# Performance work log

Hardware: AMD Instinct MI355X
Metric: run time of the kernel (lower is better)

Reference implementation:

```python
import jax, jax.numpy as jnp
import numpy as np

N_USERS = 50000
N_ENT = 100000
N_EDGES = 2_000_000
N_INTER = 1_000_000
CHANNEL = 64
N_HEADS = 2
D_K = CHANNEL // N_HEADS
N_HOPS = 2
N_REL = 10  # relation_emb has N_REL-1 rows


def setup_inputs() -> dict:
    key = jax.random.key(0)
    ks = jax.random.split(key, 8)
    user_emb = jax.random.normal(ks[0], (N_USERS, CHANNEL), jnp.float32) * 0.1
    entity_emb = jax.random.normal(ks[1], (N_ENT, CHANNEL), jnp.float32) * 0.1
    relation_emb = jax.random.normal(ks[2], (N_REL - 1, CHANNEL), jnp.float32) * 0.1
    W_Q = jax.random.normal(ks[3], (CHANNEL, CHANNEL), jnp.float32) * (1.0 / np.sqrt(CHANNEL))
    edge_index = jax.random.randint(ks[4], (2, N_EDGES), 0, N_ENT)
    edge_type = jax.random.randint(ks[5], (N_EDGES,), 1, N_REL)  # in [1, N_REL-1]
    inter_edge = jnp.stack([
        jax.random.randint(ks[6], (N_INTER,), 0, N_USERS),
        jax.random.randint(ks[7], (N_INTER,), 0, N_ENT),
    ])
    inter_edge_w = jnp.full((N_INTER,), 1.0 / 20.0, jnp.float32)
    return {
        "user_emb": user_emb,
        "entity_emb": entity_emb,
        "relation_emb": relation_emb,
        "W_Q": W_Q,
        "inter_edge_w": inter_edge_w,
        "edge_index": edge_index,
        "edge_type": edge_type,
        "inter_edge": inter_edge,
    }


def _l2norm(x):
    # F.normalize(dim=-1) with eps=1e-12
    n = jnp.linalg.norm(x, axis=-1, keepdims=True)
    return x / jnp.maximum(n, 1e-12)


def _scatter_softmax(logits, seg, num_segments):
    # per-segment (over leading axis) numerically-stable softmax; logits [E, H]
    m = jax.ops.segment_max(logits, seg, num_segments=num_segments)
    e = jnp.exp(logits - m[seg])
    s = jax.ops.segment_sum(e, seg, num_segments=num_segments)
    return e / s[seg]


def reference(user_emb, entity_emb, relation_emb, W_Q, inter_edge_w,
              edge_index, edge_type, inter_edge):
    head, tail = edge_index[0], edge_index[1]
    u_idx, i_idx = inter_edge[0], inter_edge[1]
    rel = relation_emb[edge_type - 1]  # [E, C]
    inv_sqrt_dk = 1.0 / np.sqrt(D_K)

    entity_res, user_res = entity_emb, user_emb
    for _ in range(N_HOPS):
        h_emb = entity_emb[head]                       # [E, C]
        t_emb = entity_emb[tail]                       # [E, C]
        q = (h_emb @ W_Q).reshape(-1, N_HEADS, D_K)    # [E, H, Dk]
        k = (t_emb @ W_Q).reshape(-1, N_HEADS, D_K) * rel.reshape(-1, N_HEADS, D_K)
        score = (q * k).sum(-1) * inv_sqrt_dk          # [E, H]
        attn = _scatter_softmax(score, head, N_ENT)    # [E, H]
        value = (t_emb * rel).reshape(-1, N_HEADS, D_K)
        agg = (value * attn[..., None]).reshape(-1, CHANNEL)
        entity_agg = jax.ops.segment_sum(agg, head, num_segments=N_ENT)
        item_agg = inter_edge_w[:, None] * entity_emb[i_idx]
        user_agg = jax.ops.segment_sum(item_agg, u_idx, num_segments=N_USERS)
        # mess_dropout disabled (eval mode)
        entity_emb = _l2norm(entity_agg)
        user_emb = _l2norm(user_agg)
        entity_res = entity_res + entity_emb
        user_res = user_res + user_emb
    return entity_res, user_res
```

## Files before the change

### kernel.cpp

```cpp
#include <hip/hip_runtime.h>

#define NU     50000
#define NEN    100000
#define NEDGE  2000000
#define NINTER 1000000
#define CH     64
#define NRELM1 9
#define CAPE   64
#define CAPU   64

#define BINSH   8
#define NBINE   ((NEN + 255) >> BINSH)
#define NBINU   ((NU  + 255) >> BINSH)
#define CHUNKE  4096
#define CHUNKU  2048
#define NBE_BLK ((NEDGE  + CHUNKE - 1) / CHUNKE)
#define NBU_BLK ((NINTER + CHUNKU - 1) / CHUNKU)
#define DSTRE   416
#define DSTRU   224
#define NSTR_E  ((NEN * CH) / 2048)
#define NSTR_U  ((NU * CH + 2047) / 2048)
#define NPLACE  (NBINE + NBINU)
#define NGEMM0  ((NEN + 127) / 128)
#define NGEMM   ((NEN + 63) / 64)

typedef _Float16 hv2 __attribute__((ext_vector_type(2)));
typedef _Float16 h8  __attribute__((ext_vector_type(8)));
typedef float    f32x4 __attribute__((ext_vector_type(4)));
union P4 { float4 f; hv2 h[4]; };

static __device__ __forceinline__ hv2 pkrtz(float a, float b) {
    return __builtin_bit_cast(hv2, __builtin_amdgcn_cvt_pkrtz(a, b));
}


__global__ __launch_bounds__(256) void k_bin(
    const float* __restrict__ ue, const float* __restrict__ ee,
    const float* __restrict__ re, const float* __restrict__ wq,
    const float* __restrict__ iw, const int* __restrict__ eidx,
    const int* __restrict__ etype, const int* __restrict__ ii,
    _Float16* __restrict__ QE, float* __restrict__ Eres, float* __restrict__ Ures,
    _Float16* __restrict__ Relh, _Float16* __restrict__ Wt,
    unsigned* __restrict__ dirE, unsigned* __restrict__ dirU,
    int* __restrict__ blkBufE, unsigned long long* __restrict__ blkBufU)
{
    __shared__ long long srt64[CHUNKU];
    __shared__ int hist[512];
    __shared__ int sc[512];
    __shared__ int segtot[8];
    int* srt = (int*)srt64;
    int b = blockIdx.x, tid = threadIdx.x;
    int lane63 = tid & 63, wv = tid >> 6;

    if (b < NBE_BLK) {
        hist[tid] = 0; hist[tid + 256] = 0;
        __syncthreads();
        int base = b * CHUNKE;
        int n = NEDGE - base; if (n > CHUNKE) n = CHUNKE;
        for (int i = tid; i < n; i += 256)
            atomicAdd(&hist[eidx[base + i] >> BINSH], 1);
        __syncthreads();
        {
            int v0 = hist[tid], v1 = hist[tid + 256];
            int s0 = v0, s1 = v1;
#pragma unroll
            for (int off = 1; off < 64; off <<= 1) {
                int u0 = __shfl_up(s0, off);
                int u1 = __shfl_up(s1, off);
                if (lane63 >= off) { s0 += u0; s1 += u1; }
            }
            if (lane63 == 63) { segtot[wv] = s0; segtot[4 + wv] = s1; }
            __syncthreads();
            int base0 = 0, base1 = 0;
#pragma unroll
            for (int k = 0; k < 8; ++k) {
                int t = segtot[k];
                if (k < wv)     base0 += t;
                if (k < 4 + wv) base1 += t;
            }
            sc[tid]       = base0 + s0 - v0;
            sc[tid + 256] = base1 + s1 - v1;
            __syncthreads();
        }
        for (int i = tid; i < n; i += 256) {
            int h  = eidx[base + i];
            int t  = eidx[NEDGE + base + i];
            int rt = etype[base + i] - 1;
            int pos = atomicAdd(&sc[h >> BINSH], 1);
            srt[pos] = (h & 255) | ((t | (rt << 17)) << 8);
        }
        __syncthreads();
        int4* dst = (int4*)(blkBufE + b * CHUNKE);
        const int4* s4 = (const int4*)srt;
        for (int j = tid; j < ((n + 3) >> 2); j += 256) dst[j] = s4[j];
        for (int bin = tid; bin < NBINE; bin += 256)
            dirE[b * DSTRE + bin] =
                ((unsigned)(sc[bin] - hist[bin]) << 16) | (unsigned)hist[bin];
    } else if (b < NBE_BLK + NBU_BLK) {
        hist[tid] = 0; hist[tid + 256] = 0;
        __syncthreads();
        int ub = b - NBE_BLK;
        int base = ub * CHUNKU;
        int n = NINTER - base; if (n > CHUNKU) n = CHUNKU;
        for (int i = tid; i < n; i += 256)
            atomicAdd(&hist[ii[base + i] >> BINSH], 1);
        __syncthreads();
        {
            int v0 = hist[tid], v1 = hist[tid + 256];
            int s0 = v0, s1 = v1;
#pragma unroll
            for (int off = 1; off < 64; off <<= 1) {
                int u0 = __shfl_up(s0, off);
                int u1 = __shfl_up(s1, off);
                if (lane63 >= off) { s0 += u0; s1 += u1; }
            }
            if (lane63 == 63) { segtot[wv] = s0; segtot[4 + wv] = s1; }
            __syncthreads();
            int base0 = 0, base1 = 0;
#pragma unroll
            for (int k = 0; k < 8; ++k) {
                int t = segtot[k];
                if (k < wv)     base0 += t;
                if (k < 4 + wv) base1 += t;
            }
            sc[tid]       = base0 + s0 - v0;
            sc[tid + 256] = base1 + s1 - v1;
            __syncthreads();
        }
        for (int i = tid; i < n; i += 256) {
            int u = ii[base + i];
            int e = ii[NINTER + base + i];
            unsigned w = __float_as_uint(iw[base + i]);
            int pos = atomicAdd(&sc[u >> BINSH], 1);
            srt64[pos] = (unsigned long long)((u & 255) | (e << 8))
                       | ((unsigned long long)w << 32);
        }
        __syncthreads();
        int4* dst = (int4*)(blkBufU + (size_t)ub * CHUNKU);
        const int4* s4 = (const int4*)srt64;
        for (int j = tid; j < ((n + 1) >> 1); j += 256) dst[j] = s4[j];
        for (int bin = tid; bin < NBINU; bin += 256)
            dirU[ub * DSTRU + bin] =
                ((unsigned)(sc[bin] - hist[bin]) << 16) | (unsigned)hist[bin];
    } else {
        int sb = b - (NBE_BLK + NBU_BLK);
        if (sb < NSTR_E) {
            int i0 = sb * 2048 + tid * 8;
            float4 a = *(const float4*)(ee + i0);
            float4 c = *(const float4*)(ee + i0 + 4);
            *(float4*)(Eres + i0)     = a;
            *(float4*)(Eres + i0 + 4) = c;
            P4 o;
            o.h[0] = pkrtz(a.x, a.y);
            o.h[1] = pkrtz(a.z, a.w);
            o.h[2] = pkrtz(c.x, c.y);
            o.h[3] = pkrtz(c.z, c.w);
            int node = i0 >> 6, c0 = i0 & 63;
            *(float4*)(QE + (size_t)node * 128 + c0) = o.f;
        } else if (sb < NSTR_E + NSTR_U) {
            int i0 = (sb - NSTR_E) * 2048 + tid * 8;
            if (i0 < NU * CH) {
                *(float4*)(Ures + i0)     = *(const float4*)(ue + i0);
                *(float4*)(Ures + i0 + 4) = *(const float4*)(ue + i0 + 4);
            }
        } else {
            for (int i = tid; i < NRELM1 * CH; i += 256)
                Relh[i] = (_Float16)re[i];
            for (int i = tid; i < CH * CH; i += 256)
                Wt[(i & 63) * 64 + (i >> 6)] = (_Float16)wq[i];
        }
    }
}

__global__ __launch_bounds__(512) void k_pg(
    const unsigned* __restrict__ dirE, const int* __restrict__ blkBufE,
    const unsigned* __restrict__ dirU, const unsigned long long* __restrict__ blkBufU,
    int* __restrict__ cntE, int* __restrict__ csrE,
    int* __restrict__ cntU, unsigned long long* __restrict__ csrU2,
    _Float16* __restrict__ QE, const _Float16* __restrict__ Wt)
{
    __shared__ int cnt[256];
    int b = blockIdx.x, tid = threadIdx.x;
    if (b >= NPLACE) {
        int gb = b - NPLACE;
        int w = tid >> 6, lane = tid & 63;
        int r0 = gb * 128 + w * 16;
        if (r0 >= NEN) return;
        int lr = lane & 15, lg = lane >> 4;
        const _Float16* arow = QE + (size_t)(r0 + lr) * 128 + lg * 8;
        h8 a0 = *(const h8*)(arow);
        h8 a1 = *(const h8*)(arow + 32);
#pragma unroll
        for (int ct = 0; ct < 4; ++ct) {
            const _Float16* brow = Wt + (ct * 16 + lr) * 64 + lg * 8;
            h8 b0 = *(const h8*)(brow);
            h8 b1 = *(const h8*)(brow + 32);
            f32x4 c = {0.f, 0.f, 0.f, 0.f};
            c = __builtin_amdgcn_mfma_f32_16x16x32_f16(a0, b0, c, 0, 0, 0);
            c = __builtin_amdgcn_mfma_f32_16x16x32_f16(a1, b1, c, 0, 0, 0);
#pragma unroll
            for (int r = 0; r < 4; ++r)
                QE[(size_t)(r0 + lg * 4 + r) * 128 + 64 + ct * 16 + lr] = (_Float16)c[r];
        }
        return;
    }
    if (tid < 256) cnt[tid] = 0;
    __syncthreads();
    if (b < NBINE) {
        if (tid < NBE_BLK) {
            unsigned d = dirE[tid * DSTRE + b];
            int off = d >> 16, c = d & 0xFFFF;
            const int* src = blkBufE + tid * CHUNKE + off;
            for (int i = 0; i < c; ++i) {
                int rec = src[i];
                int nl = rec & 255;
                int pos = atomicAdd(&cnt[nl], 1);
                if (pos < CAPE) csrE[((b << BINSH) + nl) * CAPE + pos] = rec >> 8;
            }
        }
        __syncthreads();
        if (tid < 256) {
            int node = (b << BINSH) + tid;
            if (node < NEN) { int c = cnt[tid]; cntE[node] = c > CAPE ? CAPE : c; }
        }
    } else {
        int ub = b - NBINE;
        if (tid < NBU_BLK) {
            unsigned d = dirU[tid * DSTRU + ub];
            int off = d >> 16, c = d & 0xFFFF;
            const unsigned long long* src = blkBufU + (size_t)tid * CHUNKU + off;
            for (int i = 0; i < c; ++i) {
                unsigned long long rec = src[i];
                int nl = (int)rec & 255;
                int pos = atomicAdd(&cnt[nl], 1);
                if (pos < CAPU)
                    csrU2[((ub << BINSH) + nl) * CAPU + pos] =
                        ((rec & 0xFFFFFFFFull) >> 8) | (rec & 0xFFFFFFFF00000000ull);
            }
        }
        __syncthreads();
        if (tid < 256) {
            int node = (ub << BINSH) + tid;
            if (node < NU) { int c = cnt[tid]; cntU[node] = c > CAPU ? CAPU : c; }
        }
    }
}

__global__ __launch_bounds__(256) void k_gemm(
    _Float16* __restrict__ QE, const _Float16* __restrict__ Wt)
{
    int w = threadIdx.x >> 6, lane = threadIdx.x & 63;
    int r0 = blockIdx.x * 64 + w * 16;
    if (r0 >= NEN) return;
    int lr = lane & 15, lg = lane >> 4;
    const _Float16* arow = QE + (size_t)(r0 + lr) * 128 + lg * 8;
    h8 a0 = *(const h8*)(arow);
    h8 a1 = *(const h8*)(arow + 32);
#pragma unroll
    for (int ct = 0; ct < 4; ++ct) {
        const _Float16* brow = Wt + (ct * 16 + lr) * 64 + lg * 8;
        h8 b0 = *(const h8*)(brow);
        h8 b1 = *(const h8*)(brow + 32);
        f32x4 c = {0.f, 0.f, 0.f, 0.f};
        c = __builtin_amdgcn_mfma_f32_16x16x32_f16(a0, b0, c, 0, 0, 0);
        c = __builtin_amdgcn_mfma_f32_16x16x32_f16(a1, b1, c, 0, 0, 0);
#pragma unroll
        for (int r = 0; r < 4; ++r)
            QE[(size_t)(r0 + lg * 4 + r) * 128 + 64 + ct * 16 + lr] = (_Float16)c[r];
    }
}

template<bool LAST>
__global__ __launch_bounds__(256) void k_fused(
    const int* __restrict__ cntE, const int* __restrict__ csrE,
    const _Float16* __restrict__ QE, const _Float16* __restrict__ Relh,
    _Float16* __restrict__ QEn, float* __restrict__ Eres,
    const int* __restrict__ cntU, const unsigned long long* __restrict__ csrU2,
    float* __restrict__ Ures)
{
    __shared__ __attribute__((aligned(16))) _Float16 RelL[NRELM1 * 72];
    int tid = threadIdx.x;
    if (tid < 72) *(float4*)(RelL + (tid >> 3) * 72 + (tid & 7) * 8)
                      = *(const float4*)(Relh + tid * 8);
    __syncthreads();

    int pair = blockIdx.x * 4 + (tid >> 6);
    int lane = tid & 63;
    int wid  = pair * 2 + (lane >> 5);
    int s = (lane >> 3) & 3, l = lane & 7;
    int c8 = l * 8;

    if (wid < NEN) {
        int row = wid;
        int cnt = cntE[row];
        int beg = row * CAPE, end = beg + cnt;
        P4 q; q.f = *(const float4*)(QE + (size_t)row * 128 + 64 + c8);
        float acc[8] = {0.f,0.f,0.f,0.f,0.f,0.f,0.f,0.f};
        float den = 0.f;

        int a0 = beg + s;
        int iA = (a0 < end) ? csrE[a0] : 0;
        int iB = (a0 + 4 < end) ? csrE[a0 + 4] : 0;
        P4 teA, ktA, rlA;
        {
            const _Float16* bA = QE + (size_t)(iA & 0x1FFFF) * 128 + c8;
            teA.f = *(const float4*)bA;
            ktA.f = *(const float4*)(bA + 64);
            rlA.f = *(const float4*)(RelL + (iA >> 17) * 72 + c8);
        }
        int nit = (cnt + 3) >> 2;
        for (int it = 0; it < nit; ++it) {
            P4 teB, ktB, rlB;
            {
                const _Float16* bB = QE + (size_t)(iB & 0x1FFFF) * 128 + c8;
                teB.f = *(const float4*)bB;
                ktB.f = *(const float4*)(bB + 64);
                rlB.f = *(const float4*)(RelL + (iB >> 17) * 72 + c8);
            }
            int a2 = a0 + (it + 2) * 4;
            int iN = (a2 < end) ? csrE[a2] : 0;
            bool act = (a0 + it * 4) < end;
            float sc = 0.f;
#pragma unroll
            for (int i = 0; i < 4; ++i) {
                hv2 km = ktA.h[i] * rlA.h[i];
                sc = __builtin_amdgcn_fdot2(q.h[i], km, sc, false);
            }
            sc += __shfl_xor(sc, 1);
            sc += __shfl_xor(sc, 2);
            float ex = exp2f(sc * 0.25503489f);
            if (!act) ex = 0.f;
            den += ex;
#pragma unroll
            for (int i = 0; i < 4; ++i) {
                hv2 vm = teA.h[i] * rlA.h[i];
                acc[2*i]   += ex * (float)vm.x;
                acc[2*i+1] += ex * (float)vm.y;
            }
            teA = teB; ktA = ktB; rlA = rlB; iB = iN;
        }
        hv2 pk[4];
#pragma unroll
        for (int i = 0; i < 4; ++i)
            pk[i] = pkrtz(acc[2*i], acc[2*i+1]);
#pragma unroll
        for (int m = 8; m <= 16; m <<= 1) {
#pragma unroll
            for (int i = 0; i < 4; ++i) {
                int v = __shfl_xor(__builtin_bit_cast(int, pk[i]), m);
                pk[i] += __builtin_bit_cast(hv2, v);
            }
            den += __shfl_xor(den, m);
        }
        float af[8];
#pragma unroll
        for (int i = 0; i < 4; ++i) { af[2*i] = (float)pk[i].x; af[2*i+1] = (float)pk[i].y; }
        float invd = (den > 0.f) ? 1.f / den : 0.f;
        float ss = 0.f;
#pragma unroll
        for (int k = 0; k < 8; ++k) { af[k] *= invd; ss += af[k] * af[k]; }
        ss += __shfl_xor(ss, 1); ss += __shfl_xor(ss, 2); ss += __shfl_xor(ss, 4);
        float inv = 1.f / fmaxf(sqrtf(ss), 1e-12f);
#pragma unroll
        for (int k = 0; k < 8; ++k) af[k] *= inv;
        if (s == 0) {
            if (!LAST) {
                P4 o;
#pragma unroll
                for (int i = 0; i < 4; ++i)
                    o.h[i] = pkrtz(af[2*i], af[2*i+1]);
                *(float4*)(QEn + (size_t)row * 128 + c8) = o.f;
            }
            float4 r0 = *(const float4*)(Eres + (size_t)row * 64 + c8);
            float4 r1 = *(const float4*)(Eres + (size_t)row * 64 + c8 + 4);
            r0.x += af[0]; r0.y += af[1]; r0.z += af[2]; r0.w += af[3];
            r1.x += af[4]; r1.y += af[5]; r1.z += af[6]; r1.w += af[7];
            *(float4*)(Eres + (size_t)row * 64 + c8)     = r0;
            *(float4*)(Eres + (size_t)row * 64 + c8 + 4) = r1;
        }
    } else {
        int row = wid - NEN;
        int cnt = cntU[row];
        int beg = row * CAPU, end = beg + cnt;
        float acc[8] = {0.f,0.f,0.f,0.f,0.f,0.f,0.f,0.f};
        int a0 = beg + s;
        unsigned long long recA = (a0 < end) ? csrU2[a0] : 0ull;
        unsigned long long recB = (a0 + 4 < end) ? csrU2[a0 + 4] : 0ull;
        P4 teA; teA.f = *(const float4*)(QE + (size_t)(unsigned)recA * 128 + c8);
        int nit = (cnt + 3) >> 2;
        for (int it = 0; it < nit; ++it) {
            P4 teB; teB.f = *(const float4*)(QE + (size_t)(unsigned)recB * 128 + c8);
            int a2 = a0 + (it + 2) * 4;
            unsigned long long recN = (a2 < end) ? csrU2[a2] : 0ull;
            float wA = __uint_as_float((unsigned)(recA >> 32));
#pragma unroll
            for (int i = 0; i < 4; ++i) {
                acc[2*i]   += wA * (float)teA.h[i].x;
                acc[2*i+1] += wA * (float)teA.h[i].y;
            }
            teA = teB; recA = recB; recB = recN;
        }
        hv2 pk[4];
#pragma unroll
        for (int i = 0; i < 4; ++i)
            pk[i] = pkrtz(acc[2*i], acc[2*i+1]);
#pragma unroll
        for (int m = 8; m <= 16; m <<= 1) {
#pragma unroll
            for (int i = 0; i < 4; ++i) {
                int v = __shfl_xor(__builtin_bit_cast(int, pk[i]), m);
                pk[i] += __builtin_bit_cast(hv2, v);
            }
        }
        float af[8];
#pragma unroll
        for (int i = 0; i < 4; ++i) { af[2*i] = (float)pk[i].x; af[2*i+1] = (float)pk[i].y; }
        float ss = 0.f;
#pragma unroll
        for (int k = 0; k < 8; ++k) ss += af[k] * af[k];
        ss += __shfl_xor(ss, 1); ss += __shfl_xor(ss, 2); ss += __shfl_xor(ss, 4);
        float inv = 1.f / fmaxf(sqrtf(ss), 1e-12f);
        if (s == 0) {
            float4 r0 = *(const float4*)(Ures + (size_t)row * 64 + c8);
            float4 r1 = *(const float4*)(Ures + (size_t)row * 64 + c8 + 4);
            r0.x += af[0] * inv; r0.y += af[1] * inv; r0.z += af[2] * inv; r0.w += af[3] * inv;
            r1.x += af[4] * inv; r1.y += af[5] * inv; r1.z += af[6] * inv; r1.w += af[7] * inv;
            *(float4*)(Ures + (size_t)row * 64 + c8)     = r0;
            *(float4*)(Ures + (size_t)row * 64 + c8 + 4) = r1;
        }
    }
}

extern "C" void kernel_launch(void* const* d_in, const int* in_sizes, int n_in,
                              void* d_out, int out_size, void* d_ws, size_t ws_size,
                              hipStream_t stream)
{
    const float* ue = (const float*)d_in[0];
    const float* ee = (const float*)d_in[1];
    const float* re = (const float*)d_in[2];
    const float* wq = (const float*)d_in[3];
    const float* iw = (const float*)d_in[4];
    const int* eidx  = (const int*)d_in[5];
    const int* etype = (const int*)d_in[6];
    const int* ii    = (const int*)d_in[7];

    float* Eres = (float*)d_out;
    float* Ures = Eres + (size_t)NEN * CH;

    _Float16* Relh = (_Float16*)d_ws;
    _Float16* Wt   = Relh + 1024;
    _Float16* QEA  = Wt + 4096;
    _Float16* QEB  = QEA + (size_t)NEN * 128;
    int* cntE      = (int*)(QEB + (size_t)NEN * 128);
    int* cntU      = cntE + NEN;
    int* csrE      = cntU + NU;
    unsigned long long* csrU2 = (unsigned long long*)(csrE + (size_t)NEN * CAPE);
    unsigned* dirE = (unsigned*)(csrU2 + (size_t)NU * CAPU);
    unsigned* dirU = dirE + NBE_BLK * DSTRE;
    int* blkBufE   = (int*)QEB;
    unsigned long long* blkBufU =
        (unsigned long long*)((char*)QEB + (size_t)NBE_BLK * CHUNKE * 4);

    k_bin<<<NBE_BLK + NBU_BLK + NSTR_E + NSTR_U + 1, 256, 0, stream>>>(
        ue, ee, re, wq, iw, eidx, etype, ii,
        QEA, Eres, Ures, Relh, Wt, dirE, dirU, blkBufE, blkBufU);
    k_pg<<<NPLACE + NGEMM0, 512, 0, stream>>>(dirE, blkBufE, dirU, blkBufU,
                                              cntE, csrE, cntU, csrU2, QEA, Wt);
    k_fused<false><<<(NEN + NU) / 8, 256, 0, stream>>>(cntE, csrE, QEA, Relh,
                                                       QEB, Eres, cntU, csrU2, Ures);
    k_gemm<<<NGEMM, 256, 0, stream>>>(QEB, Wt);
    k_fused<true><<<(NEN + NU) / 8, 256, 0, stream>>>(cntE, csrE, QEB, Relh,
                                                      QEA, Eres, cntU, csrU2, Ures);
}
```

Measured before the change: 407.6 us.

## Co-schedule hop-2 user aggregation with GEMM and restructure binning into registers

The hop-2 user aggregation moves out of the final fused kernel and runs in the same launch as the W_Q GEMM, so it overlaps with the GEMM. The last launch then handles entity rows only. The binning kernel now uses half-size chunks, keeps each thread's records in registers so the inputs are read once instead of twice, and drops the separate scan array. The placement pass has each thread walk two source blocks. The trade-off is more chunks, more directory entries and a longer serial per-thread loop during placement.

Result: slower. 422.0 us (+3.5%).

```diff
diff --git a/kernel.cpp b/kernel.cpp
--- a/kernel.cpp
+++ b/kernel.cpp
@@ -12,8 +12,8 @@
 #define BINSH   8
 #define NBINE   ((NEN + 255) >> BINSH)
 #define NBINU   ((NU  + 255) >> BINSH)
-#define CHUNKE  4096
-#define CHUNKU  2048
+#define CHUNKE  2048
+#define CHUNKU  1024
 #define NBE_BLK ((NEDGE  + CHUNKE - 1) / CHUNKE)
 #define NBU_BLK ((NINTER + CHUNKU - 1) / CHUNKU)
 #define DSTRE   416
@@ -46,102 +46,117 @@
 {
     __shared__ long long srt64[CHUNKU];
     __shared__ int hist[512];
-    __shared__ int sc[512];
     __shared__ int segtot[8];
     int* srt = (int*)srt64;
     int b = blockIdx.x, tid = threadIdx.x;
     int lane63 = tid & 63, wv = tid >> 6;
 
     if (b < NBE_BLK) {
-        hist[tid] = 0; hist[tid + 256] = 0;
-        __syncthreads();
         int base = b * CHUNKE;
         int n = NEDGE - base; if (n > CHUNKE) n = CHUNKE;
-        for (int i = tid; i < n; i += 256)
-            atomicAdd(&hist[eidx[base + i] >> BINSH], 1);
-        __syncthreads();
-        {
-            int v0 = hist[tid], v1 = hist[tid + 256];
-            int s0 = v0, s1 = v1;
-#pragma unroll
-            for (int off = 1; off < 64; off <<= 1) {
-                int u0 = __shfl_up(s0, off);
-                int u1 = __shfl_up(s1, off);
-                if (lane63 >= off) { s0 += u0; s1 += u1; }
-            }
-            if (lane63 == 63) { segtot[wv] = s0; segtot[4 + wv] = s1; }
-            __syncthreads();
-            int base0 = 0, base1 = 0;
-#pragma unroll
-            for (int k = 0; k < 8; ++k) {
-                int t = segtot[k];
-                if (k < wv)     base0 += t;
-                if (k < 4 + wv) base1 += t;
-            }
-            sc[tid]       = base0 + s0 - v0;
-            sc[tid + 256] = base1 + s1 - v1;
-            __syncthreads();
-        }
-        for (int i = tid; i < n; i += 256) {
-            int h  = eidx[base + i];
-            int t  = eidx[NEDGE + base + i];
-            int rt = etype[base + i] - 1;
-            int pos = atomicAdd(&sc[h >> BINSH], 1);
-            srt[pos] = (h & 255) | ((t | (rt << 17)) << 8);
-        }
+        bool full = (n == CHUNKE);
+        int rec[8], bn[8];
+#pragma unroll
+        for (int k = 0; k < 8; ++k) {
+            int i = tid + (k << 8);
+            bool a = full || (i < n);
+            int h  = a ? eidx[base + i] : 0;
+            int t  = a ? eidx[NEDGE + base + i] : 0;
+            int rt = a ? etype[base + i] - 1 : 0;
+            bn[k]  = a ? (h >> BINSH) : -1;
+            rec[k] = (h & 255) | ((t | (rt << 17)) << 8);
+        }
+        hist[tid] = 0; hist[tid + 256] = 0;
+        __syncthreads();
+#pragma unroll
+        for (int k = 0; k < 8; ++k)
+            if (bn[k] >= 0) atomicAdd(&hist[bn[k]], 1);
+        __syncthreads();
+        int v0 = hist[tid], v1 = hist[tid + 256];
+        int s0 = v0, s1 = v1;
+#pragma unroll
+        for (int off = 1; off < 64; off <<= 1) {
+            int u0 = __shfl_up(s0, off);
+            int u1 = __shfl_up(s1, off);
+            if (lane63 >= off) { s0 += u0; s1 += u1; }
+        }
+        if (lane63 == 63) { segtot[wv] = s0; segtot[4 + wv] = s1; }
+        __syncthreads();
+        int base0 = 0, base1 = 0;
+#pragma unroll
+        for (int k = 0; k < 8; ++k) {
+            int t = segtot[k];
+            if (k < wv)     base0 += t;
+            if (k < 4 + wv) base1 += t;
+        }
+        int off0 = base0 + s0 - v0, off1 = base1 + s1 - v1;
+        hist[tid] = off0; hist[tid + 256] = off1;
+        __syncthreads();
+#pragma unroll
+        for (int k = 0; k < 8; ++k)
+            if (bn[k] >= 0) { int pos = atomicAdd(&hist[bn[k]], 1); srt[pos] = rec[k]; }
         __syncthreads();
         int4* dst = (int4*)(blkBufE + b * CHUNKE);
         const int4* s4 = (const int4*)srt;
         for (int j = tid; j < ((n + 3) >> 2); j += 256) dst[j] = s4[j];
-        for (int bin = tid; bin < NBINE; bin += 256)
-            dirE[b * DSTRE + bin] =
-                ((unsigned)(sc[bin] - hist[bin]) << 16) | (unsigned)hist[bin];
+        if (tid < NBINE)
+            dirE[b * DSTRE + tid]       = ((unsigned)off0 << 16) | (unsigned)v0;
+        if (tid + 256 < NBINE)
+            dirE[b * DSTRE + tid + 256] = ((unsigned)off1 << 16) | (unsigned)v1;
     } else if (b < NBE_BLK + NBU_BLK) {
-        hist[tid] = 0; hist[tid + 256] = 0;
-        __syncthreads();
         int ub = b - NBE_BLK;
         int base = ub * CHUNKU;
         int n = NINTER - base; if (n > CHUNKU) n = CHUNKU;
-        for (int i = tid; i < n; i += 256)
-            atomicAdd(&hist[ii[base + i] >> BINSH], 1);
-        __syncthreads();
-        {
-            int v0 = hist[tid], v1 = hist[tid + 256];
-            int s0 = v0, s1 = v1;
-#pragma unroll
-            for (int off = 1; off < 64; off <<= 1) {
-                int u0 = __shfl_up(s0, off);
-                int u1 = __shfl_up(s1, off);
-                if (lane63 >= off) { s0 += u0; s1 += u1; }
-            }
-            if (lane63 == 63) { segtot[wv] = s0; segtot[4 + wv] = s1; }
-            __syncthreads();
-            int base0 = 0, base1 = 0;
-#pragma unroll
-            for (int k = 0; k < 8; ++k) {
-                int t = segtot[k];
-                if (k < wv)     base0 += t;
-                if (k < 4 + wv) base1 += t;
-            }
-            sc[tid]       = base0 + s0 - v0;
-            sc[tid + 256] = base1 + s1 - v1;
-            __syncthreads();
-        }
-        for (int i = tid; i < n; i += 256) {
-            int u = ii[base + i];
-            int e = ii[NINTER + base + i];
-            unsigned w = __float_as_uint(iw[base + i]);
-            int pos = atomicAdd(&sc[u >> BINSH], 1);
-            srt64[pos] = (unsigned long long)((u & 255) | (e << 8))
-                       | ((unsigned long long)w << 32);
-        }
+        bool full = (n == CHUNKU);
+        unsigned long long rec64[4]; int bn[4];
+#pragma unroll
+        for (int k = 0; k < 4; ++k) {
+            int i = tid + (k << 8);
+            bool a = full || (i < n);
+            int u = a ? ii[base + i] : 0;
+            int e = a ? ii[NINTER + base + i] : 0;
+            unsigned w = a ? __float_as_uint(iw[base + i]) : 0u;
+            bn[k] = a ? (u >> BINSH) : -1;
+            rec64[k] = (unsigned long long)((u & 255) | (e << 8))
+                     | ((unsigned long long)w << 32);
+        }
+        hist[tid] = 0; hist[tid + 256] = 0;
+        __syncthreads();
+#pragma unroll
+        for (int k = 0; k < 4; ++k)
+            if (bn[k] >= 0) atomicAdd(&hist[bn[k]], 1);
+        __syncthreads();
+        int v0 = hist[tid], v1 = hist[tid + 256];
+        int s0 = v0, s1 = v1;
+#pragma unroll
+        for (int off = 1; off < 64; off <<= 1) {
+            int u0 = __shfl_up(s0, off);
+            int u1 = __shfl_up(s1, off);
+            if (lane63 >= off) { s0 += u0; s1 += u1; }
+        }
+        if (lane63 == 63) { segtot[wv] = s0; segtot[4 + wv] = s1; }
+        __syncthreads();
+        int base0 = 0, base1 = 0;
+#pragma unroll
+        for (int k = 0; k < 8; ++k) {
+            int t = segtot[k];
+            if (k < wv)     base0 += t;
+            if (k < 4 + wv) base1 += t;
+        }
+        int off0 = base0 + s0 - v0, off1 = base1 + s1 - v1;
+        hist[tid] = off0; hist[tid + 256] = off1;
+        __syncthreads();
+#pragma unroll
+        for (int k = 0; k < 4; ++k)
+            if (bn[k] >= 0) { int pos = atomicAdd(&hist[bn[k]], 1); srt64[pos] = rec64[k]; }
         __syncthreads();
         int4* dst = (int4*)(blkBufU + (size_t)ub * CHUNKU);
         const int4* s4 = (const int4*)srt64;
         for (int j = tid; j < ((n + 1) >> 1); j += 256) dst[j] = s4[j];
-        for (int bin = tid; bin < NBINU; bin += 256)
-            dirU[ub * DSTRU + bin] =
-                ((unsigned)(sc[bin] - hist[bin]) << 16) | (unsigned)hist[bin];
+        if (tid < NBINU)
+            dirU[ub * DSTRU + tid]       = ((unsigned)off0 << 16) | (unsigned)v0;
+        if (tid + 256 < NBINU)
+            dirU[ub * DSTRU + tid + 256] = ((unsigned)off1 << 16) | (unsigned)v1;
     } else {
         int sb = b - (NBE_BLK + NBU_BLK);
         if (sb < NSTR_E) {
@@ -207,16 +222,19 @@
     if (tid < 256) cnt[tid] = 0;
     __syncthreads();
     if (b < NBINE) {
-        if (tid < NBE_BLK) {
-            unsigned d = dirE[tid * DSTRE + b];
-            int off = d >> 16, c = d & 0xFFFF;
-            const int* src = blkBufE + tid * CHUNKE + off;
-            for (int i = 0; i < c; ++i) {
-                int rec = src[i];
-                int nl = rec & 255;
-                int pos = atomicAdd(&cnt[nl], 1);
-                if (pos < CAPE) csrE[((b << BINSH) + nl) * CAPE + pos] = rec >> 8;
-            }
+        unsigned d1 = (tid < NBE_BLK)       ? dirE[tid * DSTRE + b]         : 0;
+        unsigned d2 = (tid + 512 < NBE_BLK) ? dirE[(tid + 512) * DSTRE + b] : 0;
+        int c1 = d1 & 0xFFFF, c2 = d2 & 0xFFFF;
+        const int* s1 = blkBufE + tid * CHUNKE + (d1 >> 16);
+        const int* s2 = blkBufE + (tid + 512) * CHUNKE + (d2 >> 16);
+        int m = c1 > c2 ? c1 : c2;
+        for (int i = 0; i < m; ++i) {
+            int r1 = (i < c1) ? s1[i] : -1;
+            int r2 = (i < c2) ? s2[i] : -1;
+            if (r1 >= 0) { int nl = r1 & 255; int pos = atomicAdd(&cnt[nl], 1);
+                           if (pos < CAPE) csrE[((b << BINSH) + nl) * CAPE + pos] = r1 >> 8; }
+            if (r2 >= 0) { int nl = r2 & 255; int pos = atomicAdd(&cnt[nl], 1);
+                           if (pos < CAPE) csrE[((b << BINSH) + nl) * CAPE + pos] = r2 >> 8; }
         }
         __syncthreads();
         if (tid < 256) {
@@ -225,18 +243,27 @@
         }
     } else {
         int ub = b - NBINE;
-        if (tid < NBU_BLK) {
-            unsigned d = dirU[tid * DSTRU + ub];
-            int off = d >> 16, c = d & 0xFFFF;
-            const unsigned long long* src = blkBufU + (size_t)tid * CHUNKU + off;
-            for (int i = 0; i < c; ++i) {
-                unsigned long long rec = src[i];
-                int nl = (int)rec & 255;
-                int pos = atomicAdd(&cnt[nl], 1);
+        unsigned d1 = (tid < NBU_BLK)       ? dirU[tid * DSTRU + ub]         : 0;
+        unsigned d2 = (tid + 512 < NBU_BLK) ? dirU[(tid + 512) * DSTRU + ub] : 0;
+        int c1 = d1 & 0xFFFF, c2 = d2 & 0xFFFF;
+        const unsigned long long* s1 = blkBufU + (size_t)tid * CHUNKU + (d1 >> 16);
+        const unsigned long long* s2 = blkBufU + (size_t)(tid + 512) * CHUNKU + (d2 >> 16);
+        int m = c1 > c2 ? c1 : c2;
+        for (int i = 0; i < m; ++i) {
+            if (i < c1) {
+                unsigned long long rec = s1[i];
+                int nl = (int)rec & 255; int pos = atomicAdd(&cnt[nl], 1);
                 if (pos < CAPU)
                     csrU2[((ub << BINSH) + nl) * CAPU + pos] =
                         ((rec & 0xFFFFFFFFull) >> 8) | (rec & 0xFFFFFFFF00000000ull);
             }
+            if (i < c2) {
+                unsigned long long rec = s2[i];
+                int nl = (int)rec & 255; int pos = atomicAdd(&cnt[nl], 1);
+                if (pos < CAPU)
+                    csrU2[((ub << BINSH) + nl) * CAPU + pos] =
+                        ((rec & 0xFFFFFFFFull) >> 8) | (rec & 0xFFFFFFFF00000000ull);
+            }
         }
         __syncthreads();
         if (tid < 256) {
@@ -246,32 +273,7 @@
     }
 }
 
-__global__ __launch_bounds__(256) void k_gemm(
-    _Float16* __restrict__ QE, const _Float16* __restrict__ Wt)
-{
-    int w = threadIdx.x >> 6, lane = threadIdx.x & 63;
-    int r0 = blockIdx.x * 64 + w * 16;
-    if (r0 >= NEN) return;
-    int lr = lane & 15, lg = lane >> 4;
-    const _Float16* arow = QE + (size_t)(r0 + lr) * 128 + lg * 8;
-    h8 a0 = *(const h8*)(arow);
-    h8 a1 = *(const h8*)(arow + 32);
-#pragma unroll
-    for (int ct = 0; ct < 4; ++ct) {
-        const _Float16* brow = Wt + (ct * 16 + lr) * 64 + lg * 8;
-        h8 b0 = *(const h8*)(brow);
-        h8 b1 = *(const h8*)(brow + 32);
-        f32x4 c = {0.f, 0.f, 0.f, 0.f};
-        c = __builtin_amdgcn_mfma_f32_16x16x32_f16(a0, b0, c, 0, 0, 0);
-        c = __builtin_amdgcn_mfma_f32_16x16x32_f16(a1, b1, c, 0, 0, 0);
-#pragma unroll
-        for (int r = 0; r < 4; ++r)
-            QE[(size_t)(r0 + lg * 4 + r) * 128 + 64 + ct * 16 + lr] = (_Float16)c[r];
-    }
-}
-
-template<bool LAST>
-__global__ __launch_bounds__(256) void k_fused(
+__global__ __launch_bounds__(256) void k_fused0(
     const int* __restrict__ cntE, const int* __restrict__ csrE,
     const _Float16* __restrict__ QE, const _Float16* __restrict__ Relh,
     _Float16* __restrict__ QEn, float* __restrict__ Eres,
@@ -364,13 +366,11 @@
 #pragma unroll
         for (int k = 0; k < 8; ++k) af[k] *= inv;
         if (s == 0) {
-            if (!LAST) {
-                P4 o;
-#pragma unroll
-                for (int i = 0; i < 4; ++i)
-                    o.h[i] = pkrtz(af[2*i], af[2*i+1]);
-                *(float4*)(QEn + (size_t)row * 128 + c8) = o.f;
-            }
+            P4 o;
+#pragma unroll
+            for (int i = 0; i < 4; ++i)
+                o.h[i] = pkrtz(af[2*i], af[2*i+1]);
+            *(float4*)(QEn + (size_t)row * 128 + c8) = o.f;
             float4 r0 = *(const float4*)(Eres + (size_t)row * 64 + c8);
             float4 r1 = *(const float4*)(Eres + (size_t)row * 64 + c8 + 4);
             r0.x += af[0]; r0.y += af[1]; r0.z += af[2]; r0.w += af[3];
@@ -431,6 +431,185 @@
     }
 }
 
+__global__ __launch_bounds__(256) void k_gu(
+    _Float16* __restrict__ QE, const _Float16* __restrict__ Wt,
+    const int* __restrict__ cntU, const unsigned long long* __restrict__ csrU2,
+    float* __restrict__ Ures)
+{
+    int tid = threadIdx.x;
+    if (blockIdx.x < NGEMM) {
+        int w = tid >> 6, lane = tid & 63;
+        int r0 = blockIdx.x * 64 + w * 16;
+        if (r0 >= NEN) return;
+        int lr = lane & 15, lg = lane >> 4;
+        const _Float16* arow = QE + (size_t)(r0 + lr) * 128 + lg * 8;
+        h8 a0 = *(const h8*)(arow);
+        h8 a1 = *(const h8*)(arow + 32);
+#pragma unroll
+        for (int ct = 0; ct < 4; ++ct) {
+            const _Float16* brow = Wt + (ct * 16 + lr) * 64 + lg * 8;
+            h8 b0 = *(const h8*)(brow);
+            h8 b1 = *(const h8*)(brow + 32);
+            f32x4 c = {0.f, 0.f, 0.f, 0.f};
+            c = __builtin_amdgcn_mfma_f32_16x16x32_f16(a0, b0, c, 0, 0, 0);
+            c = __builtin_amdgcn_mfma_f32_16x16x32_f16(a1, b1, c, 0, 0, 0);
+#pragma unroll
+            for (int r = 0; r < 4; ++r)
+                QE[(size_t)(r0 + lg * 4 + r) * 128 + 64 + ct * 16 + lr] = (_Float16)c[r];
+        }
+        return;
+    }
+    int pair = (blockIdx.x - NGEMM) * 4 + (tid >> 6);
+    int lane = tid & 63;
+    int row = pair * 2 + (lane >> 5);
+    int s = (lane >> 3) & 3, l = lane & 7;
+    int c8 = l * 8;
+    int cnt = cntU[row];
+    int beg = row * CAPU, end = beg + cnt;
+    float acc[8] = {0.f,0.f,0.f,0.f,0.f,0.f,0.f,0.f};
+    int a0 = beg + s;
+    unsigned long long recA = (a0 < end) ? csrU2[a0] : 0ull;
+    unsigned long long recB = (a0 + 4 < end) ? csrU2[a0 + 4] : 0ull;
+    P4 teA; teA.f = *(const float4*)(QE + (size_t)(unsigned)recA * 128 + c8);
+    int nit = (cnt + 3) >> 2;
+    for (int it = 0; it < nit; ++it) {
+        P4 teB; teB.f = *(const float4*)(QE + (size_t)(unsigned)recB * 128 + c8);
+        int a2 = a0 + (it + 2) * 4;
+        unsigned long long recN = (a2 < end) ? csrU2[a2] : 0ull;
+        float wA = __uint_as_float((unsigned)(recA >> 32));
+#pragma unroll
+        for (int i = 0; i < 4; ++i) {
+            acc[2*i]   += wA * (float)teA.h[i].x;
+            acc[2*i+1] += wA * (float)teA.h[i].y;
+        }
+        teA = teB; recA = recB; recB = recN;
+    }
+    hv2 pk[4];
+#pragma unroll
+    for (int i = 0; i < 4; ++i)
+        pk[i] = pkrtz(acc[2*i], acc[2*i+1]);
+#pragma unroll
+    for (int m = 8; m <= 16; m <<= 1) {
+#pragma unroll
+        for (int i = 0; i < 4; ++i) {
+            int v = __shfl_xor(__builtin_bit_cast(int, pk[i]), m);
+            pk[i] += __builtin_bit_cast(hv2, v);
+        }
+    }
+    float af[8];
+#pragma unroll
+    for (int i = 0; i < 4; ++i) { af[2*i] = (float)pk[i].x; af[2*i+1] = (float)pk[i].y; }
+    float ss = 0.f;
+#pragma unroll
+    for (int k = 0; k < 8; ++k) ss += af[k] * af[k];
+    ss += __shfl_xor(ss, 1); ss += __shfl_xor(ss, 2); ss += __shfl_xor(ss, 4);
+    float inv = 1.f / fmaxf(sqrtf(ss), 1e-12f);
+    if (s == 0) {
+        float4 r0 = *(const float4*)(Ures + (size_t)row * 64 + c8);
+        float4 r1 = *(const float4*)(Ures + (size_t)row * 64 + c8 + 4);
+        r0.x += af[0] * inv; r0.y += af[1] * inv; r0.z += af[2] * inv; r0.w += af[3] * inv;
+        r1.x += af[4] * inv; r1.y += af[5] * inv; r1.z += af[6] * inv; r1.w += af[7] * inv;
+        *(float4*)(Ures + (size_t)row * 64 + c8)     = r0;
+        *(float4*)(Ures + (size_t)row * 64 + c8 + 4) = r1;
+    }
+}
+
+__global__ __launch_bounds__(256) void k_fusedE(
+    const int* __restrict__ cntE, const int* __restrict__ csrE,
+    const _Float16* __restrict__ QE, const _Float16* __restrict__ Relh,
+    float* __restrict__ Eres)
+{
+    __shared__ __attribute__((aligned(16))) _Float16 RelL[NRELM1 * 72];
+    int tid = threadIdx.x;
+    if (tid < 72) *(float4*)(RelL + (tid >> 3) * 72 + (tid & 7) * 8)
+                      = *(const float4*)(Relh + tid * 8);
+    __syncthreads();
+
+    int pair = blockIdx.x * 4 + (tid >> 6);
+    int lane = tid & 63;
+    int row  = pair * 2 + (lane >> 5);
+    int s = (lane >> 3) & 3, l = lane & 7;
+    int c8 = l * 8;
+
+    int cnt = cntE[row];
+    int beg = row * CAPE, end = beg + cnt;
+    P4 q; q.f = *(const float4*)(QE + (size_t)row * 128 + 64 + c8);
+    float acc[8] = {0.f,0.f,0.f,0.f,0.f,0.f,0.f,0.f};
+    float den = 0.f;
+
+    int a0 = beg + s;
+    int iA = (a0 < end) ? csrE[a0] : 0;
+    int iB = (a0 + 4 < end) ? csrE[a0 + 4] : 0;
+    P4 teA, ktA, rlA;
+    {
+        const _Float16* bA = QE + (size_t)(iA & 0x1FFFF) * 128 + c8;
+        teA.f = *(const float4*)bA;
+        ktA.f = *(const float4*)(bA + 64);
+        rlA.f = *(const float4*)(RelL + (iA >> 17) * 72 + c8);
+    }
+    int nit = (cnt + 3) >> 2;
+    for (int it = 0; it < nit; ++it) {
+        P4 teB, ktB, rlB;
+        {
+            const _Float16* bB = QE + (size_t)(iB & 0x1FFFF) * 128 + c8;
+            teB.f = *(const float4*)bB;
+            ktB.f = *(const float4*)(bB + 64);
+            rlB.f = *(const float4*)(RelL + (iB >> 17) * 72 + c8);
+        }
+        int a2 = a0 + (it + 2) * 4;
+        int iN = (a2 < end) ? csrE[a2] : 0;
+        bool act = (a0 + it * 4) < end;
+        float sc = 0.f;
+#pragma unroll
+        for (int i = 0; i < 4; ++i) {
+            hv2 km = ktA.h[i] * rlA.h[i];
+            sc = __builtin_amdgcn_fdot2(q.h[i], km, sc, false);
+        }
+        sc += __shfl_xor(sc, 1);
+        sc += __shfl_xor(sc, 2);
+        float ex = exp2f(sc * 0.25503489f);
+        if (!act) ex = 0.f;
+        den += ex;
+#pragma unroll
+        for (int i = 0; i < 4; ++i) {
+            hv2 vm = teA.h[i] * rlA.h[i];
+            acc[2*i]   += ex * (float)vm.x;
+            acc[2*i+1] += ex * (float)vm.y;
+        }
+        teA = teB; ktA = ktB; rlA = rlB; iB = iN;
+    }
+    hv2 pk[4];
+#pragma unroll
+    for (int i = 0; i < 4; ++i)
+        pk[i] = pkrtz(acc[2*i], acc[2*i+1]);
+#pragma unroll
+    for (int m = 8; m <= 16; m <<= 1) {
+#pragma unroll
+        for (int i = 0; i < 4; ++i) {
+            int v = __shfl_xor(__builtin_bit_cast(int, pk[i]), m);
+            pk[i] += __builtin_bit_cast(hv2, v);
+        }
+        den += __shfl_xor(den, m);
+    }
+    float af[8];
+#pragma unroll
+    for (int i = 0; i < 4; ++i) { af[2*i] = (float)pk[i].x; af[2*i+1] = (float)pk[i].y; }
+    float invd = (den > 0.f) ? 1.f / den : 0.f;
+    float ss = 0.f;
+#pragma unroll
+    for (int k = 0; k < 8; ++k) { af[k] *= invd; ss += af[k] * af[k]; }
+    ss += __shfl_xor(ss, 1); ss += __shfl_xor(ss, 2); ss += __shfl_xor(ss, 4);
+    float inv = 1.f / fmaxf(sqrtf(ss), 1e-12f);
+    if (s == 0) {
+        float4 r0 = *(const float4*)(Eres + (size_t)row * 64 + c8);
+        float4 r1 = *(const float4*)(Eres + (size_t)row * 64 + c8 + 4);
+        r0.x += af[0] * inv; r0.y += af[1] * inv; r0.z += af[2] * inv; r0.w += af[3] * inv;
+        r1.x += af[4] * inv; r1.y += af[5] * inv; r1.z += af[6] * inv; r1.w += af[7] * inv;
+        *(float4*)(Eres + (size_t)row * 64 + c8)     = r0;
+        *(float4*)(Eres + (size_t)row * 64 + c8 + 4) = r1;
+    }
+}
+
 extern "C" void kernel_launch(void* const* d_in, const int* in_sizes, int n_in,
                               void* d_out, int out_size, void* d_ws, size_t ws_size,
                               hipStream_t stream)
@@ -466,9 +645,8 @@
         QEA, Eres, Ures, Relh, Wt, dirE, dirU, blkBufE, blkBufU);
     k_pg<<<NPLACE + NGEMM0, 512, 0, stream>>>(dirE, blkBufE, dirU, blkBufU,
                                               cntE, csrE, cntU, csrU2, QEA, Wt);
-    k_fused<false><<<(NEN + NU) / 8, 256, 0, stream>>>(cntE, csrE, QEA, Relh,
-                                                       QEB, Eres, cntU, csrU2, Ures);
-    k_gemm<<<NGEMM, 256, 0, stream>>>(QEB, Wt);
-    k_fused<true><<<(NEN + NU) / 8, 256, 0, stream>>>(cntE, csrE, QEB, Relh,
-                                                      QEA, Eres, cntU, csrU2, Ures);
+    k_fused0<<<(NEN + NU) / 8, 256, 0, stream>>>(cntE, csrE, QEA, Relh,
+                                                 QEB, Eres, cntU, csrU2, Ures);
+    k_gu<<<NGEMM + NU / 8, 256, 0, stream>>>(QEB, Wt, cntU, csrU2, Ures);
+    k_fusedE<<<NEN / 8, 256, 0, stream>>>(cntE, csrE, QEB, Relh, Eres);
 }
```
